# Optimization experiments

Hardware: AMD Instinct MI355X
Metric: run time of the kernel (lower is better)

## Reference

```python
import jax, jax.numpy as jnp
import numpy as np

N, D, V = 4096, 1024, 50257
CUT0, CUT1 = 2000, 10000  # head covers [0, 2000); cluster0 [2000,10000); cluster1 [10000,50257)


def setup_inputs() -> dict:
    key = jax.random.key(0)
    ks = jax.random.split(key, 8)
    hidden = jax.random.normal(ks[0], (N, D), dtype=jnp.float32)
    target = jax.random.randint(ks[1], (N,), 0, V)
    target = jnp.where(jax.random.uniform(ks[2], (N,)) < 0.05, -1, target)
    s = 0.02
    head_w = jax.random.normal(ks[3], (CUT0 + 2, D), dtype=jnp.float32) * s
    proj0 = jax.random.normal(ks[4], (256, D), dtype=jnp.float32) * s   # d_model // 4
    tail0 = jax.random.normal(ks[5], (CUT1 - CUT0, 256), dtype=jnp.float32) * s
    proj1 = jax.random.normal(ks[6], (64, D), dtype=jnp.float32) * s    # d_model // 16
    tail1 = jax.random.normal(ks[7], (V - CUT1, 64), dtype=jnp.float32) * s
    return {"hidden": hidden, "target": target, "head_w": head_w,
            "proj0": proj0, "tail0": tail0, "proj1": proj1, "tail1": tail1}


def reference(hidden, target, head_w, proj0, tail0, proj1, tail1):
    n = hidden.shape[0]
    rows = jnp.arange(n)
    valid = target >= 0
    t = jnp.clip(target, 0, V - 1)

    # Head: 2000 frequent words + 2 cluster logits
    head_lp = jax.nn.log_softmax(hidden @ head_w.T, axis=-1)  # (N, 2002)
    out = head_lp[rows, jnp.clip(t, 0, CUT0 - 1)]

    # Tail clusters: per-cluster low-rank projection + log-softmax, gather target,
    # add head log-prob of the cluster token.
    clusters = [(CUT0, CUT1, proj0, tail0, 0), (CUT1, V, proj1, tail1, 1)]
    for lo, hi, proj, tail, ci in clusters:
        rel = jnp.clip(t - lo, 0, hi - lo - 1)
        tail_lp = jax.nn.log_softmax((hidden @ proj.T) @ tail.T, axis=-1)  # (N, hi-lo)
        clus_out = head_lp[:, CUT0 + ci] + tail_lp[rows, rel]
        out = jnp.where((t >= lo) & (t < hi), clus_out, out)

    output_full = jnp.where(valid, out, jnp.zeros((), hidden.dtype))
    n_valid = jnp.sum(valid)
    denom = jnp.maximum(n_valid, 1).astype(hidden.dtype)
    loss = -jnp.sum(output_full) / denom
    loss = jnp.where(n_valid > 0, loss, jnp.zeros((), hidden.dtype))
    return output_full, loss
```

## Files before the change

kernel.cpp:

```cpp
#include <hip/hip_runtime.h>
#include <math.h>

using f32x4  = __attribute__((ext_vector_type(4))) float;
using bf16x8 = __attribute__((ext_vector_type(8))) short;

#define GLOAD_LDS16(gp, lp)                                            \
  __builtin_amdgcn_global_load_lds(                                    \
      (const __attribute__((address_space(1))) void*)(gp),             \
      (__attribute__((address_space(3))) void*)(lp), 16, 0, 0)

namespace {
constexpr int N_ROWS = 4096;
constexpr int D      = 1024;
constexpr int CUT0   = 2000, CUT1 = 10000, VTOT = 50257;
constexpr int HM   = 2002;
constexpr int HMP  = 2048;
constexpr int T0M  = 8000,              T0MP = 8000;
constexpr int T1M  = VTOT - CUT1;
constexpr int T1MP = 40272;
constexpr float LOG2E = 1.4426950408889634f;
constexpr int POS_NONE = 0x7FFFFFFF;
constexpr int POS_C1   = 1 << 30;
constexpr int SL1 = 96, SL0 = 64;
constexpr int RPB1 = 128, RPB0 = 64;
constexpr int G_T1 = (N_ROWS / RPB1) * SL1;
constexpr int G_T0 = (N_ROWS / RPB0) * SL0;
constexpr long long BH = (long long)N_ROWS * D;
constexpr long long B0 = (long long)HMP * D;
constexpr long long B1 = B0 + (long long)T0MP * 256;
constexpr long long B2 = B1 + (long long)T1MP * 64;
constexpr long long B3 = B2 + (long long)256 * D;
constexpr long long B4 = B3 + (long long)64 * D;
constexpr long long TOT = BH + B4;
constexpr int NCONV = (int)((TOT / 8 + 255) / 256);
}

__device__ __forceinline__ unsigned short f2bf(float x) {
  unsigned u = __builtin_bit_cast(unsigned, x);
  u += 0x7FFFu + ((u >> 16) & 1u);
  return (unsigned short)(u >> 16);
}
__device__ __forceinline__ float bf2f(unsigned short b) {
  unsigned u = ((unsigned)b) << 16;
  return __builtin_bit_cast(float, u);
}
__device__ __forceinline__ bf16x8 pack8(float4 f0, float4 f1, float sc) {
  bf16x8 o;
  o[0] = f2bf(f0.x * sc); o[1] = f2bf(f0.y * sc);
  o[2] = f2bf(f0.z * sc); o[3] = f2bf(f0.w * sc);
  o[4] = f2bf(f1.x * sc); o[5] = f2bf(f1.y * sc);
  o[6] = f2bf(f1.z * sc); o[7] = f2bf(f1.w * sc);
  return o;
}


__global__ __launch_bounds__(256) void prep_k(
    const float* __restrict__ hidden, const float* __restrict__ hw,
    const float* __restrict__ t0, const float* __restrict__ t1,
    const float* __restrict__ p0, const float* __restrict__ p1,
    unsigned short* __restrict__ hbf, unsigned short* __restrict__ dhw,
    unsigned short* __restrict__ dt0, unsigned short* __restrict__ dt1,
    unsigned short* __restrict__ dp0, unsigned short* __restrict__ dp1,
    const int* __restrict__ tgt, int* __restrict__ cnt,
    int* __restrict__ l0, int* __restrict__ l1, int* __restrict__ pos) {
  if (blockIdx.x == NCONV) {
    __shared__ int s0[256], s1[256];
    int tid = threadIdx.x;
    int c0 = 0, c1 = 0;
#pragma unroll
    for (int j = 0; j < 16; ++j) {
      int v = tgt[tid * 16 + j];
      c0 += (v >= CUT0 && v < CUT1);
      c1 += (v >= CUT1);
    }
    s0[tid] = c0; s1[tid] = c1;
    __syncthreads();
    for (int off = 1; off < 256; off <<= 1) {
      int a0 = (tid >= off) ? s0[tid - off] : 0;
      int a1 = (tid >= off) ? s1[tid - off] : 0;
      __syncthreads();
      s0[tid] += a0; s1[tid] += a1;
      __syncthreads();
    }
    int b0 = s0[tid] - c0, b1 = s1[tid] - c1;
#pragma unroll
    for (int j = 0; j < 16; ++j) {
      int row = tid * 16 + j;
      int v = tgt[row];
      if (v >= CUT0 && v < CUT1)      { l0[b0] = row; pos[row] = b0; ++b0; }
      else if (v >= CUT1)             { l1[b1] = row; pos[row] = b1 | POS_C1; ++b1; }
      else                            { pos[row] = POS_NONE; }
    }
    if (tid == 255) { cnt[0] = s0[255]; cnt[1] = s1[255]; }
    return;
  }
  long long i = ((long long)blockIdx.x * 256 + threadIdx.x) * 8;
  if (i >= TOT) return;
  if (i < BH) {
    int c = (int)(i >> 3);
    int row = c >> 7, k8 = c & 127;
    const float* hp = hidden + (size_t)row * D + k8 * 8;
    float4 f0 = *(const float4*)hp, f1 = *(const float4*)(hp + 4);
    bf16x8 o = pack8(f0, f1, 1.f);
    size_t tb = (size_t)(row >> 6) * 131072;
    int boff = (((row & 63) * 2048 + k8 * 16) ^ ((row & 7) << 4));
    *(bf16x8*)((char*)hbf + tb + boff) = o;
    return;
  }
  long long j = i - BH;
  const float* src; unsigned short* dst; long long off, nsrc;
  float scale = LOG2E;
  if (j < B0)      { src = hw; dst = dhw; off = j;      nsrc = (long long)HM * D; }
  else if (j < B1) { src = t0; dst = dt0; off = j - B0; nsrc = (long long)T0M * 256; }
  else if (j < B2) { src = t1; dst = dt1; off = j - B1; nsrc = (long long)T1M * 64; }
  else if (j < B3) { src = p0; dst = dp0; off = j - B2; nsrc = (long long)256 * D; scale = 1.f; }
  else             { src = p1; dst = dp1; off = j - B3; nsrc = (long long)64 * D;  scale = 1.f; }
  bf16x8 o;
  if (off < nsrc) {
    float4 f0 = *(const float4*)(src + off), f1 = *(const float4*)(src + off + 4);
    o = pack8(f0, f1, scale);
  } else {
    o = bf16x8{0, 0, 0, 0, 0, 0, 0, 0};
  }
  *(bf16x8*)(dst + off) = o;
}


__global__ __launch_bounds__(512) void headz_k(const unsigned short* __restrict__ hbf,
    const unsigned short* __restrict__ hwbf, const unsigned short* __restrict__ p0bf,
    const unsigned short* __restrict__ p1bf, const int* __restrict__ posc,
    unsigned short* __restrict__ z0, unsigned short* __restrict__ z1,
    float* __restrict__ hs_part) {
  __shared__ char Ab[64 * 2048];
  __shared__ float red[8][64];
  int rb = blockIdx.x >> 2, slice = blockIdx.x & 3;
  int tid = threadIdx.x;

  const bf16x8* src = (const bf16x8*)(hbf + (size_t)rb * 65536);
  bf16x8* dstv = (bf16x8*)Ab;
#pragma unroll
  for (int j = 0; j < 16; ++j) dstv[j * 512 + tid] = src[j * 512 + tid];
  __syncthreads();

  int w = tid >> 6, l = tid & 63, lr = l & 15, kg = l >> 4;
  int tg0 = (slice * 8 + w) * 4;
  int zt = slice * 8 + w;
  bool hasz = zt < 20;
  const unsigned short* zb = hasz
      ? (zt < 16 ? p0bf + (size_t)(zt * 16 + lr) * D
                 : p1bf + (size_t)((zt - 16) * 16 + lr) * D)
      : p0bf;
  f32x4 zero4 = {0.f, 0.f, 0.f, 0.f};
  f32x4 acc[4][4];
  f32x4 zac[4];
#pragma unroll
  for (int rg = 0; rg < 4; ++rg) {
    zac[rg] = zero4;
#pragma unroll
    for (int t = 0; t < 4; ++t) acc[rg][t] = zero4;
  }

#pragma unroll 4
  for (int kc = 0; kc < 32; ++kc) {
    bf16x8 af[4], bf[4];
#pragma unroll
    for (int rg = 0; rg < 4; ++rg) {
      int addr = ((rg * 16 + lr) * 2048 + kc * 64 + kg * 16) ^ ((lr & 7) << 4);
      af[rg] = *(const bf16x8*)(Ab + addr);
    }
#pragma unroll
    for (int t = 0; t < 4; ++t)
      bf[t] = *(const bf16x8*)(hwbf + (size_t)((tg0 + t) * 16 + lr) * D + kc * 32 + kg * 8);
#pragma unroll
    for (int rg = 0; rg < 4; ++rg)
#pragma unroll
      for (int t = 0; t < 4; ++t)
        acc[rg][t] = __builtin_amdgcn_mfma_f32_16x16x32_bf16(af[rg], bf[t], acc[rg][t], 0, 0, 0);
    if (hasz) {
      bf16x8 bz = *(const bf16x8*)(zb + kc * 32 + kg * 8);
#pragma unroll
      for (int rg = 0; rg < 4; ++rg)
        zac[rg] = __builtin_amdgcn_mfma_f32_16x16x32_bf16(af[rg], bz, zac[rg], 0, 0, 0);
    }
  }

  float sv[4][4];
#pragma unroll
  for (int rg = 0; rg < 4; ++rg)
#pragma unroll
    for (int v = 0; v < 4; ++v) {
      float s = 0.f;
#pragma unroll
      for (int t = 0; t < 4; ++t) s += __builtin_amdgcn_exp2f(acc[rg][t][v]);
      sv[rg][v] = s;
    }
#pragma unroll
  for (int off = 1; off < 16; off <<= 1)
#pragma unroll
    for (int rg = 0; rg < 4; ++rg)
#pragma unroll
      for (int v = 0; v < 4; ++v) sv[rg][v] += __shfl_xor(sv[rg][v], off);
  if (lr == 0)
#pragma unroll
    for (int rg = 0; rg < 4; ++rg)
#pragma unroll
      for (int v = 0; v < 4; ++v) red[w][rg * 16 + kg * 4 + v] = sv[rg][v];

  if (hasz) {
#pragma unroll
    for (int rg = 0; rg < 4; ++rg)
#pragma unroll
      for (int v = 0; v < 4; ++v) {
        int grow = rb * 64 + rg * 16 + kg * 4 + v;
        int pcv = posc[grow];
        if (zt < 16) {
          if (pcv < POS_C1)
            z0[(size_t)pcv * 256 + zt * 16 + lr] = f2bf(zac[rg][v]);
        } else {
          if (pcv != POS_NONE && pcv >= POS_C1)
            z1[(size_t)(pcv & (POS_C1 - 1)) * 64 + (zt - 16) * 16 + lr] = f2bf(zac[rg][v]);
        }
      }
  }
  __syncthreads();
  if (tid < 64) {
    float s = 0.f;
#pragma unroll
    for (int ww = 0; ww < 8; ++ww) s += red[ww][tid];
    hs_part[slice * N_ROWS + rb * 64 + tid] = s;
  }
}


__device__ __forceinline__ void tail1_body(int bid, const unsigned short* __restrict__ z,
    const unsigned short* __restrict__ twbf, const int* __restrict__ list,
    const int* __restrict__ cntp, float* __restrict__ ts_part,
    char* __restrict__ Bl) {
  constexpr int MT = T1MP / 16;
  constexpr int ST = (MT + SL1 - 1) / SL1;
  int n = *cntp;
  int rowblock = bid / SL1, slice = bid % SL1;
  int rowbase = rowblock * RPB1;
  if (rowbase >= n) return;
  int t0 = slice * ST, t1e = min(t0 + ST, MT);
  if (t0 >= t1e) return;
  int tid = threadIdx.x, w = tid >> 6, l = tid & 63, lr = l & 15, kg = l >> 4;

  bf16x8 a[2][2];
#pragma unroll
  for (int rg = 0; rg < 2; ++rg) {
    int idx = min(rowbase + w * 32 + rg * 16 + lr, n - 1);
    const unsigned short* zp = z + (size_t)idx * 64 + kg * 8;
    a[rg][0] = *(const bf16x8*)(zp);
    a[rg][1] = *(const bf16x8*)(zp + 32);
  }

  int sb = tid * 16;
  int stile = sb >> 11, scol = (sb >> 7) & 15;
  int sbyte = (sb & 127) ^ ((scol & 7) << 4);
  const char* tb = (const char*)twbf;
  int mtm1 = MT - 1;
  auto stage = [&](int gt, int buf) {
    int tA = min(gt + stile, mtm1);
    GLOAD_LDS16(tb + (size_t)tA * 2048 + scol * 128 + sbyte, Bl + buf * 4096 + sb);
  };

  int NG = (t1e - t0 + 1) >> 1;
  stage(t0, 0);
  __syncthreads();

  float s[2][4] = {};
  f32x4 zero4 = {0.f, 0.f, 0.f, 0.f};
  int rd0 = (lr * 128 + kg * 16) ^ ((lr & 7) << 4);
  int cur = 0;
  for (int g = 0; g < NG; ++g) {
    int gt = t0 + g * 2;
    if (g + 1 < NG) stage(gt + 2, cur ^ 1);
#pragma unroll
    for (int t = 0; t < 2; ++t) {
      if (gt + t < t1e) {
        const char* bb = Bl + cur * 4096 + t * 2048;
        bf16x8 b0 = *(const bf16x8*)(bb + rd0);
        bf16x8 b1 = *(const bf16x8*)(bb + (rd0 ^ 64));
        f32x4 acc0 = __builtin_amdgcn_mfma_f32_16x16x32_bf16(a[0][0], b0, zero4, 0, 0, 0);
        f32x4 acc1 = __builtin_amdgcn_mfma_f32_16x16x32_bf16(a[1][0], b0, zero4, 0, 0, 0);
        acc0 = __builtin_amdgcn_mfma_f32_16x16x32_bf16(a[0][1], b1, acc0, 0, 0, 0);
        acc1 = __builtin_amdgcn_mfma_f32_16x16x32_bf16(a[1][1], b1, acc1, 0, 0, 0);
#pragma unroll
        for (int v = 0; v < 4; ++v) {
          s[0][v] += __builtin_amdgcn_exp2f(acc0[v]);
          s[1][v] += __builtin_amdgcn_exp2f(acc1[v]);
        }
      }
    }
    __syncthreads();
    cur ^= 1;
  }

#pragma unroll
  for (int off = 1; off < 16; off <<= 1)
#pragma unroll
    for (int rg = 0; rg < 2; ++rg)
#pragma unroll
      for (int v = 0; v < 4; ++v) s[rg][v] += __shfl_xor(s[rg][v], off);
  if (lr == 0) {
#pragma unroll
    for (int rg = 0; rg < 2; ++rg)
#pragma unroll
      for (int v = 0; v < 4; ++v) {
        int idx = rowbase + w * 32 + rg * 16 + kg * 4 + v;
        if (idx < n)
          ts_part[(size_t)slice * N_ROWS + list[idx]] = s[rg][v];
      }
  }
}

__device__ __forceinline__ void tail0_body(int bid, const unsigned short* __restrict__ z,
    const unsigned short* __restrict__ twbf, const int* __restrict__ list,
    const int* __restrict__ cntp, float* __restrict__ ts_part,
    char* __restrict__ Bl) {
  constexpr int MT = T0MP / 16;
  constexpr int ST = (MT + SL0 - 1) / SL0;
  int n = *cntp;
  int rowblock = bid / SL0, slice = bid % SL0;
  int rowbase = rowblock * RPB0;
  if (rowbase >= n) return;
  int t0 = slice * ST, t1e = min(t0 + ST, MT);
  if (t0 >= t1e) return;
  int tid = threadIdx.x, w = tid >> 6, l = tid & 63, lr = l & 15, kg = l >> 4;

  bf16x8 a[8];
  {
    int idx = min(rowbase + w * 16 + lr, n - 1);
    const unsigned short* zp = z + (size_t)idx * 256 + kg * 8;
#pragma unroll
    for (int kc = 0; kc < 8; ++kc) a[kc] = *(const bf16x8*)(zp + kc * 32);
  }

  int sb0 = tid * 16, sb1 = sb0 + 4096;
  int c0s = sb0 >> 9, b0s = (sb0 & 511) ^ ((c0s & 7) << 4);
  int c1s = sb1 >> 9, b1s = (sb1 & 511) ^ ((c1s & 7) << 4);
  const char* tb = (const char*)twbf;
  auto stage = [&](int gt, int buf) {
    GLOAD_LDS16(tb + (size_t)gt * 8192 + c0s * 512 + b0s, Bl + buf * 8192 + sb0);
    GLOAD_LDS16(tb + (size_t)gt * 8192 + c1s * 512 + b1s, Bl + buf * 8192 + sb1);
  };

  int NG = t1e - t0;
  stage(t0, 0);
  __syncthreads();

  float s[4] = {};
  f32x4 zero4 = {0.f, 0.f, 0.f, 0.f};
  int swz = (lr & 7) << 4;
  int rdb = lr * 512 + kg * 16;
  int cur = 0;
  for (int g = 0; g < NG; ++g) {
    if (g + 1 < NG) stage(t0 + g + 1, cur ^ 1);
    const char* bb = Bl + cur * 8192;
    f32x4 acc = zero4;
#pragma unroll
    for (int kc = 0; kc < 8; ++kc) {
      bf16x8 b = *(const bf16x8*)(bb + ((rdb + kc * 64) ^ swz));
      acc = __builtin_amdgcn_mfma_f32_16x16x32_bf16(a[kc], b, acc, 0, 0, 0);
    }
#pragma unroll
    for (int v = 0; v < 4; ++v) s[v] += __builtin_amdgcn_exp2f(acc[v]);
    __syncthreads();
    cur ^= 1;
  }

#pragma unroll
  for (int off = 1; off < 16; off <<= 1)
#pragma unroll
    for (int v = 0; v < 4; ++v) s[v] += __shfl_xor(s[v], off);
  if (lr == 0) {
#pragma unroll
    for (int v = 0; v < 4; ++v) {
      int idx = rowbase + w * 16 + kg * 4 + v;
      if (idx < n)
        ts_part[(size_t)slice * N_ROWS + list[idx]] = s[v];
    }
  }
}

__global__ __launch_bounds__(256, 8) void tf_k(
    const unsigned short* __restrict__ z0, const unsigned short* __restrict__ t0bf,
    const unsigned short* __restrict__ z1, const unsigned short* __restrict__ t1bf,
    const int* __restrict__ l0, const int* __restrict__ l1,
    const int* __restrict__ cnt, float* __restrict__ ts0_part,
    float* __restrict__ ts1_part) {
  __shared__ char Bl[16384];
  int b = blockIdx.x;
  if (b < G_T1)
    tail1_body(b, z1, t1bf, l1, cnt + 1, ts1_part, Bl);
  else
    tail0_body(b - G_T1, z0, t0bf, l0, cnt + 0, ts0_part, Bl);
}


__global__ __launch_bounds__(256) void finalize_k(const float* __restrict__ hidden,
    const int* __restrict__ tgt, const float* __restrict__ head_w,
    const float* __restrict__ tail0, const float* __restrict__ tail1,
    const unsigned short* __restrict__ z0, const unsigned short* __restrict__ z1,
    const int* __restrict__ pos, const float* __restrict__ hs_part,
    const float* __restrict__ ts0_part, const float* __restrict__ ts1_part,
    float* __restrict__ out) {
  int w = threadIdx.x >> 6, l = threadIdx.x & 63;
  int row = blockIdx.x * 4 + w;
  int t = tgt[row];
  int jt = t < 0 ? 0 : (t < CUT0 ? t : (t < CUT1 ? CUT0 : CUT0 + 1));
  const float4* h4 = (const float4*)(hidden + (size_t)row * D);
  const float4* w4 = (const float4*)(head_w + (size_t)jt * D);
  float acc = 0.f;
#pragma unroll
  for (int j = 0; j < 4; ++j) {
    float4 a = h4[l + 64 * j], b = w4[l + 64 * j];
    acc += a.x * b.x + a.y * b.y + a.z * b.z + a.w * b.w;
  }
  float hp = (l < 4) ? hs_part[l * N_ROWS + row] : 0.f;
#pragma unroll
  for (int off = 32; off; off >>= 1) {
    acc += __shfl_xor(acc, off);
    hp  += __shfl_xor(hp, off);
  }
  float val = acc - __logf(hp - 46.f);
  if (t >= CUT0) {
    int p = pos[row] & (POS_C1 - 1);
    float ta = 0.f, tp = 0.f;
    if (t < CUT1) {
      const unsigned short* zr = z0 + (size_t)p * 256;
      const float* tw = tail0 + (size_t)(t - CUT0) * 256;
#pragma unroll
      for (int j = 0; j < 4; ++j) ta += bf2f(zr[l + 64 * j]) * tw[l + 64 * j];
      tp = ts0_part[(size_t)l * N_ROWS + row];
    } else {
      const unsigned short* zr = z1 + (size_t)p * 64;
      const float* tw = tail1 + (size_t)(t - CUT1) * 64;
      ta = bf2f(zr[l]) * tw[l];
      tp = ts1_part[(size_t)l * N_ROWS + row];
      if (l < SL1 - 64) tp += ts1_part[(size_t)(64 + l) * N_ROWS + row];
    }
#pragma unroll
    for (int off = 32; off; off >>= 1) {
      ta += __shfl_xor(ta, off);
      tp += __shfl_xor(tp, off);
    }
    float lt = tp - ((t >= CUT1) ? 15.f : 0.f);
    val += ta - __logf(lt);
  }
  if (l == 0) out[row] = (t < 0) ? 0.f : val;
}


__global__ __launch_bounds__(256) void loss_k(const float* __restrict__ out,
                                              const int* __restrict__ target,
                                              float* __restrict__ loss) {
  __shared__ float ssum[256];
  __shared__ int scnt[256];
  float s = 0.f; int c = 0;
  for (int i = threadIdx.x; i < N_ROWS; i += 256) {
    s += out[i];
    if (target[i] >= 0) c++;
  }
  ssum[threadIdx.x] = s; scnt[threadIdx.x] = c;
  __syncthreads();
  for (int off = 128; off; off >>= 1) {
    if (threadIdx.x < off) {
      ssum[threadIdx.x] += ssum[threadIdx.x + off];
      scnt[threadIdx.x] += scnt[threadIdx.x + off];
    }
    __syncthreads();
  }
  if (threadIdx.x == 0) {
    int nv = scnt[0];
    loss[0] = (nv > 0) ? (-ssum[0] / (float)nv) : 0.f;
  }
}


extern "C" void kernel_launch(void* const* d_in, const int* in_sizes, int n_in,
                              void* d_out, int out_size, void* d_ws, size_t ws_size,
                              hipStream_t stream) {
  const float* hidden = (const float*)d_in[0];
  const int*   target = (const int*)d_in[1];
  const float* head_w = (const float*)d_in[2];
  const float* proj0  = (const float*)d_in[3];
  const float* tail0  = (const float*)d_in[4];
  const float* proj1  = (const float*)d_in[5];
  const float* tail1  = (const float*)d_in[6];
  float* out = (float*)d_out;

  char* wp = (char*)d_ws;
  auto alloc = [&](size_t bytes) {
    char* p = wp;
    wp += (bytes + 255) & ~(size_t)255;
    return p;
  };
  int* cnt   = (int*)alloc(8);
  int* list0 = (int*)alloc(N_ROWS * 4);
  int* list1 = (int*)alloc(N_ROWS * 4);
  int* pos   = (int*)alloc(N_ROWS * 4);
  unsigned short* hbf  = (unsigned short*)alloc((size_t)N_ROWS * D * 2);
  unsigned short* hwbf = (unsigned short*)alloc((size_t)HMP * D * 2);
  unsigned short* t0bf = (unsigned short*)alloc((size_t)T0MP * 256 * 2);
  unsigned short* t1bf = (unsigned short*)alloc((size_t)T1MP * 64 * 2);
  unsigned short* p0bf = (unsigned short*)alloc((size_t)256 * D * 2);
  unsigned short* p1bf = (unsigned short*)alloc((size_t)64 * D * 2);
  unsigned short* z0   = (unsigned short*)alloc((size_t)N_ROWS * 256 * 2);
  unsigned short* z1   = (unsigned short*)alloc((size_t)N_ROWS * 64 * 2);
  float* hs_part  = (float*)alloc((size_t)4 * N_ROWS * 4);
  float* ts0_part = (float*)alloc((size_t)SL0 * N_ROWS * 4);
  float* ts1_part = (float*)alloc((size_t)SL1 * N_ROWS * 4);

  prep_k<<<NCONV + 1, 256, 0, stream>>>(hidden, head_w, tail0, tail1, proj0, proj1,
                                        hbf, hwbf, t0bf, t1bf, p0bf, p1bf,
                                        target, cnt, list0, list1, pos);
  headz_k<<<(N_ROWS / 64) * 4, 512, 0, stream>>>(hbf, hwbf, p0bf, p1bf, pos,
                                                 z0, z1, hs_part);
  tf_k<<<G_T1 + G_T0, 256, 0, stream>>>(z0, t0bf, z1, t1bf, list0, list1, cnt,
                                        ts0_part, ts1_part);
  finalize_k<<<N_ROWS / 4, 256, 0, stream>>>(hidden, target, head_w, tail0, tail1,
                                             z0, z1, pos, hs_part, ts0_part, ts1_part, out);
  loss_k<<<1, 256, 0, stream>>>(out, target, out + N_ROWS);
}
```

Before: 109.2 us.

## Restructure head GEMM: 16 column slices, register-held A, double-buffered LDS B tiles

Rewrites the head/projection GEMM kernel so each block covers 64 rows and a 128-column slice (16 slices instead of 4), using 256 threads. The hidden-state A fragments are now read straight from global memory into registers per 256-wide K chunk. The head-weight B tiles are staged into double-buffered LDS via async global-to-LDS loads, replacing the 128KB LDS copy of A and the direct global reads of B. The aim is to shrink LDS use and raise occupancy and block count, overlapping weight loads with MFMA. In exchange, the head partial-sum buffer grows to 16 partials per row, and each tile step adds a block-wide barrier.

```diff
diff --git a/kernel.cpp b/kernel.cpp
--- a/kernel.cpp
+++ b/kernel.cpp
@@ -21,6 +21,8 @@
 constexpr float LOG2E = 1.4426950408889634f;
 constexpr int POS_NONE = 0x7FFFFFFF;
 constexpr int POS_C1   = 1 << 30;
+constexpr int HSL = 16;
+constexpr int G_HK = (N_ROWS / 64) * HSL;
 constexpr int SL1 = 96, SL0 = 64;
 constexpr int RPB1 = 128, RPB0 = 64;
 constexpr int G_T1 = (N_ROWS / RPB1) * SL1;
@@ -126,108 +128,103 @@
 }
 
 
-__global__ __launch_bounds__(512) void headz_k(const unsigned short* __restrict__ hbf,
+__global__ __launch_bounds__(256) void headk_k(const unsigned short* __restrict__ hbf,
     const unsigned short* __restrict__ hwbf, const unsigned short* __restrict__ p0bf,
     const unsigned short* __restrict__ p1bf, const int* __restrict__ posc,
     unsigned short* __restrict__ z0, unsigned short* __restrict__ z1,
     float* __restrict__ hs_part) {
-  __shared__ char Ab[64 * 2048];
-  __shared__ float red[8][64];
-  int rb = blockIdx.x >> 2, slice = blockIdx.x & 3;
-  int tid = threadIdx.x;
-
-  const bf16x8* src = (const bf16x8*)(hbf + (size_t)rb * 65536);
-  bf16x8* dstv = (bf16x8*)Ab;
-#pragma unroll
-  for (int j = 0; j < 16; ++j) dstv[j * 512 + tid] = src[j * 512 + tid];
+  __shared__ char Bl[16384];
+  int rb = blockIdx.x >> 4, slice = blockIdx.x & 15;
+  int tid = threadIdx.x, w = tid >> 6, l = tid & 63, lr = l & 15, kg = l >> 4;
+  int row = rb * 64 + w * 16 + lr;
+
+  int sb0 = tid * 16, sb1 = sb0 + 4096;
+  int c0s = sb0 >> 9, b0s = (sb0 & 511) ^ ((c0s & 7) << 4);
+  int c1s = sb1 >> 9, b1s = (sb1 & 511) ^ ((c1s & 7) << 4);
+  const char* wb = (const char*)hwbf;
+  int colbase = slice * 128;
+  auto stage = [&](int p, int buf) {
+    int c = p >> 3, t = p & 7;
+    const char* src = wb + (size_t)(colbase + t * 16) * 2048 + c * 512;
+    GLOAD_LDS16(src + (size_t)c0s * 2048 + b0s, Bl + buf * 8192 + sb0);
+    GLOAD_LDS16(src + (size_t)c1s * 2048 + b1s, Bl + buf * 8192 + sb1);
+  };
+
+  const char* ab = (const char*)hbf + (size_t)rb * 131072;
+  int r63 = row & 63, rsw = (row & 7) << 4;
+
+  const unsigned short* zbA = p0bf + (size_t)(slice * 16 + lr) * D;
+  bool hasB = slice < 4;
+  const unsigned short* zbB = hasB ? p1bf + (size_t)(slice * 16 + lr) * D : p0bf;
+
+  f32x4 zero4 = {0.f, 0.f, 0.f, 0.f};
+  f32x4 acc[8];
+  f32x4 zacA = zero4, zacB = zero4;
+#pragma unroll
+  for (int t = 0; t < 8; ++t) acc[t] = zero4;
+
+  int swz = (lr & 7) << 4;
+  int rdb = lr * 512 + kg * 16;
+
+  stage(0, 0);
   __syncthreads();
-
-  int w = tid >> 6, l = tid & 63, lr = l & 15, kg = l >> 4;
-  int tg0 = (slice * 8 + w) * 4;
-  int zt = slice * 8 + w;
-  bool hasz = zt < 20;
-  const unsigned short* zb = hasz
-      ? (zt < 16 ? p0bf + (size_t)(zt * 16 + lr) * D
-                 : p1bf + (size_t)((zt - 16) * 16 + lr) * D)
-      : p0bf;
-  f32x4 zero4 = {0.f, 0.f, 0.f, 0.f};
-  f32x4 acc[4][4];
-  f32x4 zac[4];
-#pragma unroll
-  for (int rg = 0; rg < 4; ++rg) {
-    zac[rg] = zero4;
-#pragma unroll
-    for (int t = 0; t < 4; ++t) acc[rg][t] = zero4;
-  }
-
-#pragma unroll 4
-  for (int kc = 0; kc < 32; ++kc) {
-    bf16x8 af[4], bf[4];
-#pragma unroll
-    for (int rg = 0; rg < 4; ++rg) {
-      int addr = ((rg * 16 + lr) * 2048 + kc * 64 + kg * 16) ^ ((lr & 7) << 4);
-      af[rg] = *(const bf16x8*)(Ab + addr);
-    }
-#pragma unroll
-    for (int t = 0; t < 4; ++t)
-      bf[t] = *(const bf16x8*)(hwbf + (size_t)((tg0 + t) * 16 + lr) * D + kc * 32 + kg * 8);
-#pragma unroll
-    for (int rg = 0; rg < 4; ++rg)
-#pragma unroll
-      for (int t = 0; t < 4; ++t)
-        acc[rg][t] = __builtin_amdgcn_mfma_f32_16x16x32_bf16(af[rg], bf[t], acc[rg][t], 0, 0, 0);
-    if (hasz) {
-      bf16x8 bz = *(const bf16x8*)(zb + kc * 32 + kg * 8);
-#pragma unroll
-      for (int rg = 0; rg < 4; ++rg)
-        zac[rg] = __builtin_amdgcn_mfma_f32_16x16x32_bf16(af[rg], bz, zac[rg], 0, 0, 0);
-    }
-  }
-
-  float sv[4][4];
-#pragma unroll
-  for (int rg = 0; rg < 4; ++rg)
-#pragma unroll
-    for (int v = 0; v < 4; ++v) {
-      float s = 0.f;
-#pragma unroll
-      for (int t = 0; t < 4; ++t) s += __builtin_amdgcn_exp2f(acc[rg][t][v]);
-      sv[rg][v] = s;
-    }
+  int cur = 0;
+  for (int c = 0; c < 4; ++c) {
+    bf16x8 a[8];
+#pragma unroll
+    for (int kc = 0; kc < 8; ++kc) {
+      int k8 = c * 32 + kc * 4 + kg;
+      a[kc] = *(const bf16x8*)(ab + ((r63 * 2048 + k8 * 16) ^ rsw));
+    }
+#pragma unroll
+    for (int t = 0; t < 8; ++t) {
+      int p = c * 8 + t;
+      if (p + 1 < 32) stage(p + 1, cur ^ 1);
+      const char* bb = Bl + cur * 8192;
+#pragma unroll
+      for (int kc = 0; kc < 8; ++kc) {
+        bf16x8 b = *(const bf16x8*)(bb + ((rdb + kc * 64) ^ swz));
+        acc[t] = __builtin_amdgcn_mfma_f32_16x16x32_bf16(a[kc], b, acc[t], 0, 0, 0);
+      }
+      __syncthreads();
+      cur ^= 1;
+    }
+#pragma unroll
+    for (int kc = 0; kc < 8; ++kc) {
+      bf16x8 bz = *(const bf16x8*)(zbA + c * 256 + kc * 32 + kg * 8);
+      zacA = __builtin_amdgcn_mfma_f32_16x16x32_bf16(a[kc], bz, zacA, 0, 0, 0);
+    }
+    if (hasB) {
+#pragma unroll
+      for (int kc = 0; kc < 8; ++kc) {
+        bf16x8 bz = *(const bf16x8*)(zbB + c * 256 + kc * 32 + kg * 8);
+        zacB = __builtin_amdgcn_mfma_f32_16x16x32_bf16(a[kc], bz, zacB, 0, 0, 0);
+      }
+    }
+  }
+
+  float s[4] = {};
+#pragma unroll
+  for (int t = 0; t < 8; ++t)
+#pragma unroll
+    for (int v = 0; v < 4; ++v) s[v] += __builtin_amdgcn_exp2f(acc[t][v]);
 #pragma unroll
   for (int off = 1; off < 16; off <<= 1)
 #pragma unroll
-    for (int rg = 0; rg < 4; ++rg)
-#pragma unroll
-      for (int v = 0; v < 4; ++v) sv[rg][v] += __shfl_xor(sv[rg][v], off);
-  if (lr == 0)
-#pragma unroll
-    for (int rg = 0; rg < 4; ++rg)
-#pragma unroll
-      for (int v = 0; v < 4; ++v) red[w][rg * 16 + kg * 4 + v] = sv[rg][v];
-
-  if (hasz) {
-#pragma unroll
-    for (int rg = 0; rg < 4; ++rg)
-#pragma unroll
-      for (int v = 0; v < 4; ++v) {
-        int grow = rb * 64 + rg * 16 + kg * 4 + v;
-        int pcv = posc[grow];
-        if (zt < 16) {
-          if (pcv < POS_C1)
-            z0[(size_t)pcv * 256 + zt * 16 + lr] = f2bf(zac[rg][v]);
-        } else {
-          if (pcv != POS_NONE && pcv >= POS_C1)
-            z1[(size_t)(pcv & (POS_C1 - 1)) * 64 + (zt - 16) * 16 + lr] = f2bf(zac[rg][v]);
-        }
-      }
-  }
-  __syncthreads();
-  if (tid < 64) {
-    float s = 0.f;
-#pragma unroll
-    for (int ww = 0; ww < 8; ++ww) s += red[ww][tid];
-    hs_part[slice * N_ROWS + rb * 64 + tid] = s;
+    for (int v = 0; v < 4; ++v) s[v] += __shfl_xor(s[v], off);
+  if (lr == 0) {
+#pragma unroll
+    for (int v = 0; v < 4; ++v)
+      hs_part[(size_t)slice * N_ROWS + rb * 64 + w * 16 + kg * 4 + v] = s[v];
+  }
+#pragma unroll
+  for (int v = 0; v < 4; ++v) {
+    int grow = rb * 64 + w * 16 + kg * 4 + v;
+    int pcv = posc[grow];
+    if (pcv < POS_C1)
+      z0[(size_t)pcv * 256 + slice * 16 + lr] = f2bf(zacA[v]);
+    if (hasB && pcv != POS_NONE && pcv >= POS_C1)
+      z1[(size_t)(pcv & (POS_C1 - 1)) * 64 + slice * 16 + lr] = f2bf(zacB[v]);
   }
 }
 
@@ -418,7 +415,7 @@
     float4 a = h4[l + 64 * j], b = w4[l + 64 * j];
     acc += a.x * b.x + a.y * b.y + a.z * b.z + a.w * b.w;
   }
-  float hp = (l < 4) ? hs_part[l * N_ROWS + row] : 0.f;
+  float hp = (l < HSL) ? hs_part[(size_t)l * N_ROWS + row] : 0.f;
 #pragma unroll
   for (int off = 32; off; off >>= 1) {
     acc += __shfl_xor(acc, off);
@@ -509,15 +506,14 @@
   unsigned short* p1bf = (unsigned short*)alloc((size_t)64 * D * 2);
   unsigned short* z0   = (unsigned short*)alloc((size_t)N_ROWS * 256 * 2);
   unsigned short* z1   = (unsigned short*)alloc((size_t)N_ROWS * 64 * 2);
-  float* hs_part  = (float*)alloc((size_t)4 * N_ROWS * 4);
+  float* hs_part  = (float*)alloc((size_t)HSL * N_ROWS * 4);
   float* ts0_part = (float*)alloc((size_t)SL0 * N_ROWS * 4);
   float* ts1_part = (float*)alloc((size_t)SL1 * N_ROWS * 4);
 
   prep_k<<<NCONV + 1, 256, 0, stream>>>(hidden, head_w, tail0, tail1, proj0, proj1,
                                         hbf, hwbf, t0bf, t1bf, p0bf, p1bf,
                                         target, cnt, list0, list1, pos);
-  headz_k<<<(N_ROWS / 64) * 4, 512, 0, stream>>>(hbf, hwbf, p0bf, p1bf, pos,
-                                                 z0, z1, hs_part);
+  headk_k<<<G_HK, 256, 0, stream>>>(hbf, hwbf, p0bf, p1bf, pos, z0, z1, hs_part);
   tf_k<<<G_T1 + G_T0, 256, 0, stream>>>(z0, t0bf, z1, t1bf, list0, list1, cnt,
                                         ts0_part, ts1_part);
   finalize_k<<<N_ROWS / 4, 256, 0, stream>>>(hidden, target, head_w, tail0, tail1,
```

After: 124.0 us. 13.5% more time.
